# Kernel tuning notes

Hardware: AMD Instinct MI355X
Metric: run time of the kernel (lower is better)

## Reference

```python
import jax, jax.numpy as jnp
import numpy as np
import math

HIDDEN = 1024
NUM_HEADS = 16
HEAD_DIM = HIDDEN // NUM_HEADS


def _rope_tables(seq_len, dim, dtype):
    inv_freq = 1.0 / (10000.0 ** (np.arange(0, dim, 2, dtype=np.float32) / dim))
    t = np.arange(seq_len, dtype=np.float32)
    freqs = np.einsum('i,j->ij', t, inv_freq)          # [S, dim/2]
    emb = np.concatenate([freqs, freqs], axis=-1)      # [S, dim]
    return jnp.asarray(np.cos(emb), dtype), jnp.asarray(np.sin(emb), dtype)


def _rotate_half(x):
    x1, x2 = x[..., : x.shape[-1] // 2], x[..., x.shape[-1] // 2:]
    return jnp.concatenate([-x2, x1], axis=-1)


def setup_inputs() -> dict:
    key = jax.random.key(0)
    k1, k2, k3 = jax.random.split(key, 3)
    B, S = 2, 2048
    x = jax.random.normal(k1, (B, S, HIDDEN), dtype=jnp.float32)
    attention_mask = jnp.ones((B, S), dtype=jnp.int32)
    w_qkv = jax.random.normal(k2, (HIDDEN, 3 * HIDDEN), dtype=jnp.float32) * (1.0 / math.sqrt(HIDDEN))
    w_out = jax.random.normal(k3, (HIDDEN, HIDDEN), dtype=jnp.float32) * (1.0 / math.sqrt(HIDDEN))
    return {"x": x, "attention_mask": attention_mask, "w_qkv": w_qkv, "w_out": w_out}


def reference(x, attention_mask, w_qkv, w_out):
    B, S, H = x.shape
    qkv = x @ w_qkv                                   # [B,S,3H]
    qkv = qkv.reshape(B, S, NUM_HEADS, 3 * HEAD_DIM).transpose(0, 2, 1, 3)  # [B,h,S,3d]
    q, k, v = jnp.split(qkv, 3, axis=-1)              # each [B,h,S,d]
    cos, sin = _rope_tables(S, HEAD_DIM, x.dtype)     # [S,d]
    cos = cos[None, None]
    sin = sin[None, None]
    q = q * cos + _rotate_half(q) * sin
    k = k * cos + _rotate_half(k) * sin
    scale = math.sqrt(HEAD_DIM)
    scores = jnp.einsum('bhqd,bhkd->bhqk', q, k) / scale  # [B,h,S,S]
    mask_value = jnp.finfo(scores.dtype).min
    scores = jnp.where(attention_mask[:, None, None, :] == 0, mask_value, scores)
    attn = jax.nn.softmax(scores, axis=-1)
    context = jnp.einsum('bhqk,bhkd->bhqd', attn, v)  # [B,h,S,d]
    context = context.transpose(0, 2, 1, 3).reshape(B, S, H)
    return context @ w_out
```

## Files before the change

### kernel.cpp

```cpp
#include <hip/hip_runtime.h>
#include <hip/hip_bf16.h>
#include <math.h>
#include <stdint.h>


typedef __bf16 bf16;
typedef __bf16 bf16x8 __attribute__((ext_vector_type(8)));
typedef __bf16 bf16x4 __attribute__((ext_vector_type(4)));
typedef float f32x4 __attribute__((ext_vector_type(4)));

#define AS1 __attribute__((address_space(1)))
#define AS3 __attribute__((address_space(3)))

__device__ __forceinline__ void gload_lds16(const void* g, void* l) {
  __builtin_amdgcn_global_load_lds((const AS1 void*)g, (AS3 void*)l, 16, 0, 0);
}

__device__ __forceinline__ f32x4 mfma16(bf16x8 a, bf16x8 b, f32x4 c) {
  return __builtin_amdgcn_mfma_f32_16x16x32_bf16(a, b, c, 0, 0, 0);
}

#define S_LEN 2048
#define QSCALE 0.1803368801111144f


__global__ void k_split_x(const float* __restrict__ x, bf16* __restrict__ xh,
                          bf16* __restrict__ xl) {
  int i = blockIdx.x * 256 + threadIdx.x;
  float4 v = ((const float4*)x)[i];
  float vv[4] = {v.x, v.y, v.z, v.w};
  bf16x4 h, l;
#pragma unroll
  for (int j = 0; j < 4; j++) {
    bf16 hb = (bf16)vv[j];
    h[j] = hb;
    l[j] = (bf16)(vv[j] - (float)hb);
  }
  ((bf16x4*)xh)[i] = h;
  ((bf16x4*)xl)[i] = l;
}

__global__ void k_wt_qkv(const float* __restrict__ w, bf16* __restrict__ bth,
                         bf16* __restrict__ btl) {
  __shared__ float t[32][33];
  int n0 = blockIdx.x * 32, k0 = blockIdx.y * 32;
  int tx = threadIdx.x & 31, ty = threadIdx.x >> 5;
#pragma unroll
  for (int i = 0; i < 4; i++)
    t[ty + 8 * i][tx] = w[(size_t)(k0 + ty + 8 * i) * 3072 + n0 + tx];
  __syncthreads();
#pragma unroll
  for (int i = 0; i < 4; i++) {
    int r = ty + 8 * i;
    float v = t[tx][r];
    size_t o = (size_t)(n0 + r) * 1024 + k0 + tx;
    bf16 hb = (bf16)v;
    bth[o] = hb;
    btl[o] = (bf16)(v - (float)hb);
  }
}

__global__ void k_wt_out(const float* __restrict__ w, bf16* __restrict__ bt) {
  __shared__ float t[32][33];
  int n0 = blockIdx.x * 32, k0 = blockIdx.y * 32;
  int tx = threadIdx.x & 31, ty = threadIdx.x >> 5;
#pragma unroll
  for (int i = 0; i < 4; i++)
    t[ty + 8 * i][tx] = w[(size_t)(k0 + ty + 8 * i) * 1024 + n0 + tx];
  __syncthreads();
#pragma unroll
  for (int i = 0; i < 4; i++) {
    int r = ty + 8 * i;
    bt[(size_t)(n0 + r) * 1024 + k0 + tx] = (bf16)t[tx][r];
  }
}

__global__ void k_rope_tables(float* __restrict__ ct, float* __restrict__ st) {
  int i = blockIdx.x * 256 + threadIdx.x;
  int s = i >> 5, j = i & 31;
  double invf = pow(10000.0, -(double)j / 32.0);
  double a = (double)s * invf;
  ct[i] = (float)cos(a);
  st[i] = (float)sin(a);
}

__global__ __launch_bounds__(256, 2) void k_gemm_qkv(
    const bf16* __restrict__ Ah, const bf16* __restrict__ Al,
    const bf16* __restrict__ Bh, const bf16* __restrict__ Bl,
    bf16* __restrict__ C) {
  const int K = 1024, N = 3072;
  __shared__ __align__(16) bf16 sAh[128 * 32];
  __shared__ __align__(16) bf16 sAl[128 * 32];
  __shared__ __align__(16) bf16 sBh[128 * 32];
  __shared__ __align__(16) bf16 sBl[128 * 32];
  int tid = threadIdx.x, lane = tid & 63, wid = tid >> 6;
  int m0 = blockIdx.x * 128, n0 = blockIdx.y * 128;
  int wm = wid >> 1, wn = wid & 1;

  f32x4 acc[4][4];
#pragma unroll
  for (int a = 0; a < 4; a++)
#pragma unroll
    for (int b = 0; b < 4; b++) acc[a][b] = (f32x4){0.f, 0.f, 0.f, 0.f};

  for (int k0 = 0; k0 < K; k0 += 32) {
#pragma unroll
    for (int p = 0; p < 2; p++) {
      int slot = p * 256 + tid;
      int row = slot >> 2, c16 = slot & 3;
      int cs = c16 ^ ((row >> 1) & 3);
      int ldsoff = (p * 256 + wid * 64) * 16;
      size_t ga = (size_t)(m0 + row) * K + k0 + cs * 8;
      size_t gb = (size_t)(n0 + row) * K + k0 + cs * 8;
      gload_lds16(Ah + ga, (char*)sAh + ldsoff);
      gload_lds16(Al + ga, (char*)sAl + ldsoff);
      gload_lds16(Bh + gb, (char*)sBh + ldsoff);
      gload_lds16(Bl + gb, (char*)sBl + ldsoff);
    }
    __syncthreads();

    bf16x8 fah[4], fal[4], fbh[4], fbl[4];
#pragma unroll
    for (int mf = 0; mf < 4; mf++) {
      int row = wm * 64 + mf * 16 + (lane & 15);
      int c16 = (lane >> 4) ^ ((row >> 1) & 3);
      int off = row * 64 + c16 * 16;
      fah[mf] = *(const bf16x8*)((const char*)sAh + off);
      fal[mf] = *(const bf16x8*)((const char*)sAl + off);
    }
#pragma unroll
    for (int nf = 0; nf < 4; nf++) {
      int row = wn * 64 + nf * 16 + (lane & 15);
      int c16 = (lane >> 4) ^ ((row >> 1) & 3);
      int off = row * 64 + c16 * 16;
      fbh[nf] = *(const bf16x8*)((const char*)sBh + off);
      fbl[nf] = *(const bf16x8*)((const char*)sBl + off);
    }
#pragma unroll
    for (int mf = 0; mf < 4; mf++)
#pragma unroll
      for (int nf = 0; nf < 4; nf++) {
        acc[mf][nf] = mfma16(fah[mf], fbh[nf], acc[mf][nf]);
        acc[mf][nf] = mfma16(fah[mf], fbl[nf], acc[mf][nf]);
        acc[mf][nf] = mfma16(fal[mf], fbh[nf], acc[mf][nf]);
      }
    __syncthreads();
  }

#pragma unroll
  for (int mf = 0; mf < 4; mf++)
#pragma unroll
    for (int nf = 0; nf < 4; nf++)
#pragma unroll
      for (int r = 0; r < 4; r++) {
        int row = m0 + wm * 64 + mf * 16 + (lane >> 4) * 4 + r;
        int col = n0 + wn * 64 + nf * 16 + (lane & 15);
        C[(size_t)row * N + col] = (bf16)acc[mf][nf][r];
      }
}

__global__ void k_rope_scatter(const bf16* __restrict__ QKV,
                               const float* __restrict__ ct,
                               const float* __restrict__ st,
                               bf16* __restrict__ Q, bf16* __restrict__ Kb,
                               bf16* __restrict__ Vt) {
  __shared__ __align__(16) bf16 vt[64 * 64];
  int sblk = blockIdx.x, bh = blockIdx.y;
  int b = bh >> 4, h = bh & 15;
  int tid = threadIdx.x;
  int r = tid >> 2, c = tid & 3;
  int s = sblk * 64 + r;
  size_t rowbase = ((size_t)(b * S_LEN + s)) * 3072 + h * 192;

  bf16x8 qlo = *(const bf16x8*)(QKV + rowbase + c * 8);
  bf16x8 qhi = *(const bf16x8*)(QKV + rowbase + c * 8 + 32);
  bf16x8 klo = *(const bf16x8*)(QKV + rowbase + 64 + c * 8);
  bf16x8 khi = *(const bf16x8*)(QKV + rowbase + 64 + c * 8 + 32);
  bf16x8 vlo = *(const bf16x8*)(QKV + rowbase + 128 + c * 8);
  bf16x8 vhi = *(const bf16x8*)(QKV + rowbase + 128 + c * 8 + 32);

  bf16x8 qol, qoh, kol, koh;
#pragma unroll
  for (int j = 0; j < 8; j++) {
    float cs = ct[s * 32 + c * 8 + j], sn = st[s * 32 + c * 8 + j];
    float q1 = (float)qlo[j], q2 = (float)qhi[j];
    qol[j] = (bf16)((q1 * cs - q2 * sn) * QSCALE);
    qoh[j] = (bf16)((q2 * cs + q1 * sn) * QSCALE);
    float k1 = (float)klo[j], k2 = (float)khi[j];
    kol[j] = (bf16)(k1 * cs - k2 * sn);
    koh[j] = (bf16)(k2 * cs + k1 * sn);
  }
  size_t qb = ((size_t)bh * S_LEN + s) * 64 + c * 8;
  *(bf16x8*)(Q + qb) = qol;
  *(bf16x8*)(Q + qb + 32) = qoh;
  *(bf16x8*)(Kb + qb) = kol;
  *(bf16x8*)(Kb + qb + 32) = koh;

#pragma unroll
  for (int j = 0; j < 8; j++) {
    vt[(c * 8 + j) * 64 + r] = vlo[j];
    vt[(c * 8 + 32 + j) * 64 + r] = vhi[j];
  }
  __syncthreads();
  int d = tid >> 2, cc = tid & 3;
  size_t vb = ((size_t)bh * 64 + d) * S_LEN + sblk * 64 + cc * 16;
  *(bf16x8*)(Vt + vb) = *(const bf16x8*)(vt + d * 64 + cc * 16);
  *(bf16x8*)(Vt + vb + 8) = *(const bf16x8*)(vt + d * 64 + cc * 16 + 8);
}

__global__ __launch_bounds__(256, 2) void k_attn(
    const bf16* __restrict__ Q, const bf16* __restrict__ Kb,
    const bf16* __restrict__ Vt, const int* __restrict__ mask,
    bf16* __restrict__ Ctx) {
  __shared__ __align__(16) char sK[2][16384];
  __shared__ __align__(16) char sV[16384];
  int tid = threadIdx.x, lane = tid & 63, w = tid >> 6;
  int g = lane >> 4, q = lane & 15;
  int bh = blockIdx.x, qt = blockIdx.y;
  int b = bh >> 4, h = bh & 15;
  int q0 = qt * 128 + w * 32;

  bf16x8 bQ[2][2];
#pragma unroll
  for (int mf = 0; mf < 2; mf++)
#pragma unroll
    for (int ks = 0; ks < 2; ks++)
      bQ[mf][ks] = *(const bf16x8*)(Q + ((size_t)bh * S_LEN + q0 + mf * 16 + q) * 64 +
                                    ks * 32 + g * 8);

  f32x4 O[2][4];
  float mrow[2], lrow[2];
#pragma unroll
  for (int mf = 0; mf < 2; mf++) {
#pragma unroll
    for (int nd = 0; nd < 4; nd++) O[mf][nd] = (f32x4){0.f, 0.f, 0.f, 0.f};
    mrow[mf] = -3e38f;
    lrow[mf] = 0.f;
  }

  const bf16* kbase = Kb + (size_t)bh * S_LEN * 64;
  const bf16* vbase = Vt + (size_t)bh * 64 * S_LEN;

#pragma unroll
  for (int p = 0; p < 4; p++) {
    int slot = p * 256 + tid;
    int row = slot >> 3, c16 = slot & 7;
    int cs = c16 ^ (row & 7);
    gload_lds16(kbase + (size_t)row * 64 + cs * 8, sK[0] + (p * 256 + w * 64) * 16);
  }
  bf16x8 vst[4];
#pragma unroll
  for (int p = 0; p < 4; p++) {
    int slot = p * 256 + tid;
    int row = slot >> 4, c16 = slot & 15;
    int cs = c16 ^ (row & 7);
    vst[p] = *(const bf16x8*)(vbase + (size_t)row * S_LEN + cs * 8);
  }
#pragma unroll
  for (int p = 0; p < 4; p++)
    *(bf16x8*)(sV + (p * 256 + tid) * 16) = vst[p];
  __syncthreads();

  int db = 0;
  for (int kt = 0; kt < 16; kt++) {
    int k0 = kt * 128;
    if (kt < 15) {
#pragma unroll
      for (int p = 0; p < 4; p++) {
        int slot = p * 256 + tid;
        int row = slot >> 3, c16 = slot & 7;
        int cs = c16 ^ (row & 7);
        gload_lds16(kbase + (size_t)((kt + 1) * 128 + row) * 64 + cs * 8,
                    sK[db ^ 1] + (p * 256 + w * 64) * 16);
      }
#pragma unroll
      for (int p = 0; p < 4; p++) {
        int slot = p * 256 + tid;
        int row = slot >> 4, c16 = slot & 15;
        int cs = c16 ^ (row & 7);
        vst[p] = *(const bf16x8*)(vbase + (size_t)row * S_LEN + (kt + 1) * 128 + cs * 8);
      }
    }
    const char* kl = sK[db];

    f32x4 sfr[2][8];
#pragma unroll
    for (int mf = 0; mf < 2; mf++)
#pragma unroll
      for (int kf = 0; kf < 8; kf++) sfr[mf][kf] = (f32x4){0.f, 0.f, 0.f, 0.f};
#pragma unroll
    for (int kf = 0; kf < 8; kf++) {
#pragma unroll
      for (int ks = 0; ks < 2; ks++) {
        int row = kf * 16 + q;
        int c16 = (ks * 4 + g) ^ (row & 7);
        bf16x8 ak = *(const bf16x8*)(kl + row * 128 + c16 * 16);
        sfr[0][kf] = mfma16(ak, bQ[0][ks], sfr[0][kf]);
        sfr[1][kf] = mfma16(ak, bQ[1][ks], sfr[1][kf]);
      }
    }
    {
      int2 mv = *(const int2*)(mask + b * S_LEN + k0 + lane * 2);
      if (!__all(mv.x & mv.y)) {
#pragma unroll
        for (int kf = 0; kf < 8; kf++) {
          int4 m4 = *(const int4*)(mask + b * S_LEN + k0 + kf * 16 + g * 4);
          int mm[4] = {m4.x, m4.y, m4.z, m4.w};
#pragma unroll
          for (int r = 0; r < 4; r++)
            if (mm[r] == 0) { sfr[0][kf][r] = -1e30f; sfr[1][kf][r] = -1e30f; }
        }
      }
    }
#pragma unroll
    for (int mf = 0; mf < 2; mf++) {
      float mx = -3e38f;
#pragma unroll
      for (int kf = 0; kf < 8; kf++)
#pragma unroll
        for (int r = 0; r < 4; r++) mx = fmaxf(mx, sfr[mf][kf][r]);
      mx = fmaxf(mx, __shfl_xor(mx, 16, 64));
      mx = fmaxf(mx, __shfl_xor(mx, 32, 64));
      if (__any(mx > mrow[mf] + 8.0f)) {
        float mnew = fmaxf(mrow[mf], mx);
        float al = exp2f(mrow[mf] - mnew);
        mrow[mf] = mnew;
        lrow[mf] *= al;
#pragma unroll
        for (int nd = 0; nd < 4; nd++)
#pragma unroll
          for (int r = 0; r < 4; r++) O[mf][nd][r] *= al;
      }
      float ps = 0.f;
#pragma unroll
      for (int kf = 0; kf < 8; kf++)
#pragma unroll
        for (int r = 0; r < 4; r++) {
          float p0 = exp2f(sfr[mf][kf][r] - mrow[mf]);
          sfr[mf][kf][r] = p0;
          ps += p0;
        }
      ps += __shfl_xor(ps, 16, 64);
      ps += __shfl_xor(ps, 32, 64);
      lrow[mf] += ps;
    }

#pragma unroll
    for (int ks = 0; ks < 4; ks++) {
      bf16x8 pb[2];
#pragma unroll
      for (int mf = 0; mf < 2; mf++)
#pragma unroll
        for (int j = 0; j < 8; j++)
          pb[mf][j] = (bf16)sfr[mf][2 * ks + (j >> 2)][j & 3];
#pragma unroll
      for (int nd = 0; nd < 4; nd++) {
        int row = nd * 16 + q;
        int u1 = (ks * 4 + (g >> 1)) ^ (row & 7);
        int u2 = (ks * 4 + (g >> 1) + 2) ^ (row & 7);
        const char* vr = sV + row * 256 + ((g & 1) << 3);
        bf16x4 v0 = *(const bf16x4*)(vr + (u1 << 4));
        bf16x4 v1 = *(const bf16x4*)(vr + (u2 << 4));
        bf16x8 av;
#pragma unroll
        for (int j = 0; j < 4; j++) { av[j] = v0[j]; av[4 + j] = v1[j]; }
        O[0][nd] = mfma16(av, pb[0], O[0][nd]);
        O[1][nd] = mfma16(av, pb[1], O[1][nd]);
      }
    }
    __syncthreads();
    if (kt < 15) {
#pragma unroll
      for (int p = 0; p < 4; p++)
        *(bf16x8*)(sV + (p * 256 + tid) * 16) = vst[p];
    }
    __syncthreads();
    db ^= 1;
  }

#pragma unroll
  for (int mf = 0; mf < 2; mf++) {
    float inv = 1.f / lrow[mf];
    int srow = q0 + mf * 16 + q;
#pragma unroll
    for (int nd = 0; nd < 4; nd++) {
      bf16x4 o4;
#pragma unroll
      for (int r = 0; r < 4; r++) o4[r] = (bf16)(O[mf][nd][r] * inv);
      *(bf16x4*)(Ctx + ((size_t)b * S_LEN + srow) * 1024 + h * 64 + nd * 16 + g * 4) = o4;
    }
  }
}

__global__ __launch_bounds__(256, 2) void k_gemm_out(
    const bf16* __restrict__ A, const bf16* __restrict__ Bt,
    float* __restrict__ C) {
  const int K = 1024, N = 1024;
  __shared__ __align__(16) bf16 sA[128 * 32];
  __shared__ __align__(16) bf16 sB[128 * 32];
  int tid = threadIdx.x, lane = tid & 63, wid = tid >> 6;
  int m0 = blockIdx.x * 128, n0 = blockIdx.y * 128;
  int wm = wid >> 1, wn = wid & 1;

  f32x4 acc[4][4];
#pragma unroll
  for (int a = 0; a < 4; a++)
#pragma unroll
    for (int b = 0; b < 4; b++) acc[a][b] = (f32x4){0.f, 0.f, 0.f, 0.f};

  for (int k0 = 0; k0 < K; k0 += 32) {
#pragma unroll
    for (int p = 0; p < 2; p++) {
      int slot = p * 256 + tid;
      int row = slot >> 2, c16 = slot & 3;
      int cs = c16 ^ ((row >> 1) & 3);
      int ldsoff = (p * 256 + wid * 64) * 16;
      gload_lds16(A + (size_t)(m0 + row) * K + k0 + cs * 8, (char*)sA + ldsoff);
      gload_lds16(Bt + (size_t)(n0 + row) * K + k0 + cs * 8, (char*)sB + ldsoff);
    }
    __syncthreads();
    bf16x8 fa[4], fb[4];
#pragma unroll
    for (int mf = 0; mf < 4; mf++) {
      int row = wm * 64 + mf * 16 + (lane & 15);
      int c16 = (lane >> 4) ^ ((row >> 1) & 3);
      fa[mf] = *(const bf16x8*)((const char*)sA + row * 64 + c16 * 16);
    }
#pragma unroll
    for (int nf = 0; nf < 4; nf++) {
      int row = wn * 64 + nf * 16 + (lane & 15);
      int c16 = (lane >> 4) ^ ((row >> 1) & 3);
      fb[nf] = *(const bf16x8*)((const char*)sB + row * 64 + c16 * 16);
    }
#pragma unroll
    for (int mf = 0; mf < 4; mf++)
#pragma unroll
      for (int nf = 0; nf < 4; nf++)
        acc[mf][nf] = mfma16(fa[mf], fb[nf], acc[mf][nf]);
    __syncthreads();
  }
#pragma unroll
  for (int mf = 0; mf < 4; mf++)
#pragma unroll
    for (int nf = 0; nf < 4; nf++)
#pragma unroll
      for (int r = 0; r < 4; r++) {
        int row = m0 + wm * 64 + mf * 16 + (lane >> 4) * 4 + r;
        int col = n0 + wn * 64 + nf * 16 + (lane & 15);
        C[(size_t)row * N + col] = acc[mf][nf][r];
      }
}

extern "C" void kernel_launch(void* const* d_in, const int* in_sizes, int n_in,
                              void* d_out, int out_size, void* d_ws, size_t ws_size,
                              hipStream_t stream) {
  const float* x = (const float*)d_in[0];
  const int* mask = (const int*)d_in[1];
  const float* wqkv = (const float*)d_in[2];
  const float* wout = (const float*)d_in[3];
  float* out = (float*)d_out;
  char* ws = (char*)d_ws;

  bf16* Xh  = (bf16*)(ws + 0);
  bf16* Xl  = (bf16*)(ws + 8388608);
  bf16* Wqh = (bf16*)(ws + 16777216);
  bf16* Wql = (bf16*)(ws + 23068672);
  bf16* Wo  = (bf16*)(ws + 29360128);
  bf16* QKV = (bf16*)(ws + 31457280);
  bf16* Qb  = (bf16*)(ws + 56623104);
  bf16* Kb  = (bf16*)(ws + 65011712);
  bf16* Vt  = (bf16*)(ws + 73400320);
  bf16* Ctx = (bf16*)(ws + 81788928);
  float* ct = (float*)(ws + 90177536);
  float* st = (float*)(ws + 90439680);

  k_split_x<<<4096, 256, 0, stream>>>(x, Xh, Xl);
  k_wt_qkv<<<dim3(96, 32), 256, 0, stream>>>(wqkv, Wqh, Wql);
  k_wt_out<<<dim3(32, 32), 256, 0, stream>>>(wout, Wo);
  k_rope_tables<<<256, 256, 0, stream>>>(ct, st);
  k_gemm_qkv<<<dim3(32, 24), 256, 0, stream>>>(Xh, Xl, Wqh, Wql, QKV);
  k_rope_scatter<<<dim3(32, 32), 256, 0, stream>>>(QKV, ct, st, Qb, Kb, Vt);
  k_attn<<<dim3(32, 16), 256, 0, stream>>>(Qb, Kb, Vt, mask, Ctx);
  k_gemm_out<<<dim3(32, 8), 256, 0, stream>>>(Ctx, Wo, out);
}
```

Measured before the change: 259.8 us.

## Double-buffer V tile in attention, hoist LDS offsets and mask check

The attention kernel now double-buffers the V tile in shared memory alongside K. This removes one __syncthreads per key tile, since the next V tile is written into the other buffer. LDS read offsets and global load pointers are precomputed once, and the all-ones mask test is done once per block instead of every tile. The rope table kernel is also switched from double to float math. The cost is 64KB of LDS per block, which may limit the two-blocks-per-CU occupancy on the hardware, plus more registers held for the offset tables.

Result: no change. 259.5 us (-0.1%).

```diff
diff --git a/kernel.cpp b/kernel.cpp
--- a/kernel.cpp
+++ b/kernel.cpp
@@ -78,10 +78,10 @@
 __global__ void k_rope_tables(float* __restrict__ ct, float* __restrict__ st) {
   int i = blockIdx.x * 256 + threadIdx.x;
   int s = i >> 5, j = i & 31;
-  double invf = pow(10000.0, -(double)j / 32.0);
-  double a = (double)s * invf;
-  ct[i] = (float)cos(a);
-  st[i] = (float)sin(a);
+  float invf = powf(10000.0f, -(float)j / 32.0f);
+  float a = (float)s * invf;
+  ct[i] = cosf(a);
+  st[i] = sinf(a);
 }
 
 __global__ __launch_bounds__(256, 2) void k_gemm_qkv(
@@ -212,8 +212,9 @@
     const bf16* __restrict__ Q, const bf16* __restrict__ Kb,
     const bf16* __restrict__ Vt, const int* __restrict__ mask,
     bf16* __restrict__ Ctx) {
-  __shared__ __align__(16) char sK[2][16384];
-  __shared__ __align__(16) char sV[16384];
+  __shared__ __align__(16) char sKV[65536];
+  char* sKbase = sKV;
+  char* sVbase = sKV + 32768;
   int tid = threadIdx.x, lane = tid & 63, w = tid >> 6;
   int g = lane >> 4, q = lane & 15;
   int bh = blockIdx.x, qt = blockIdx.y;
@@ -238,15 +239,62 @@
     lrow[mf] = 0.f;
   }
 
+  bool rowall;
+  {
+    int acc = -1;
+    const int4* mr = (const int4*)(mask + (size_t)b * S_LEN) + lane * 8;
+#pragma unroll
+    for (int p = 0; p < 8; p++) {
+      int4 m4 = mr[p];
+      acc &= m4.x & m4.y & m4.z & m4.w;
+    }
+    rowall = __all(acc != 0);
+  }
+
   const bf16* kbase = Kb + (size_t)bh * S_LEN * 64;
   const bf16* vbase = Vt + (size_t)bh * 64 * S_LEN;
+
+  const bf16* kgp[4];
+  const bf16* vgp[4];
+  int kldo[4], vldo[4];
+#pragma unroll
+  for (int p = 0; p < 4; p++) {
+    int slot = p * 256 + tid;
+    int krow = slot >> 3, kc = slot & 7;
+    int kcs = kc ^ (krow & 7);
+    kgp[p] = kbase + (size_t)(128 + krow) * 64 + kcs * 8;
+    kldo[p] = (p * 256 + w * 64) * 16;
+    int vrow = slot >> 4, vc = slot & 15;
+    int vcs = vc ^ (vrow & 7);
+    vgp[p] = vbase + (size_t)vrow * S_LEN + 128 + vcs * 8;
+    vldo[p] = (p * 256 + tid) * 16;
+  }
+  int koff[8][2];
+#pragma unroll
+  for (int kf = 0; kf < 8; kf++)
+#pragma unroll
+    for (int ks = 0; ks < 2; ks++) {
+      int row = kf * 16 + q;
+      koff[kf][ks] = row * 128 + (((ks * 4 + g) ^ (row & 7)) << 4);
+    }
+  int voff[4][4][2];
+#pragma unroll
+  for (int ks = 0; ks < 4; ks++)
+#pragma unroll
+    for (int nd = 0; nd < 4; nd++) {
+      int row = nd * 16 + q;
+      int u1 = (ks * 4 + (g >> 1)) ^ (row & 7);
+      int u2 = (ks * 4 + (g >> 1) + 2) ^ (row & 7);
+      voff[ks][nd][0] = row * 256 + ((g & 1) << 3) + (u1 << 4);
+      voff[ks][nd][1] = row * 256 + ((g & 1) << 3) + (u2 << 4);
+    }
 
 #pragma unroll
   for (int p = 0; p < 4; p++) {
     int slot = p * 256 + tid;
     int row = slot >> 3, c16 = slot & 7;
     int cs = c16 ^ (row & 7);
-    gload_lds16(kbase + (size_t)row * 64 + cs * 8, sK[0] + (p * 256 + w * 64) * 16);
+    gload_lds16(kbase + (size_t)row * 64 + cs * 8, sKbase + kldo[p]);
   }
   bf16x8 vst[4];
 #pragma unroll
@@ -258,30 +306,26 @@
   }
 #pragma unroll
   for (int p = 0; p < 4; p++)
-    *(bf16x8*)(sV + (p * 256 + tid) * 16) = vst[p];
+    *(bf16x8*)(sVbase + vldo[p]) = vst[p];
   __syncthreads();
 
   int db = 0;
   for (int kt = 0; kt < 16; kt++) {
-    int k0 = kt * 128;
     if (kt < 15) {
+      char* kdst = sKbase + (db ^ 1) * 16384;
 #pragma unroll
       for (int p = 0; p < 4; p++) {
-        int slot = p * 256 + tid;
-        int row = slot >> 3, c16 = slot & 7;
-        int cs = c16 ^ (row & 7);
-        gload_lds16(kbase + (size_t)((kt + 1) * 128 + row) * 64 + cs * 8,
-                    sK[db ^ 1] + (p * 256 + w * 64) * 16);
+        gload_lds16(kgp[p], kdst + kldo[p]);
+        kgp[p] += 128 * 64;
       }
 #pragma unroll
       for (int p = 0; p < 4; p++) {
-        int slot = p * 256 + tid;
-        int row = slot >> 4, c16 = slot & 15;
-        int cs = c16 ^ (row & 7);
-        vst[p] = *(const bf16x8*)(vbase + (size_t)row * S_LEN + (kt + 1) * 128 + cs * 8);
-      }
-    }
-    const char* kl = sK[db];
+        vst[p] = *(const bf16x8*)vgp[p];
+        vgp[p] += 128;
+      }
+    }
+    const char* kl = sKbase + db * 16384;
+    const char* vl = sVbase + db * 16384;
 
     f32x4 sfr[2][8];
 #pragma unroll
@@ -292,24 +336,20 @@
     for (int kf = 0; kf < 8; kf++) {
 #pragma unroll
       for (int ks = 0; ks < 2; ks++) {
-        int row = kf * 16 + q;
-        int c16 = (ks * 4 + g) ^ (row & 7);
-        bf16x8 ak = *(const bf16x8*)(kl + row * 128 + c16 * 16);
+        bf16x8 ak = *(const bf16x8*)(kl + koff[kf][ks]);
         sfr[0][kf] = mfma16(ak, bQ[0][ks], sfr[0][kf]);
         sfr[1][kf] = mfma16(ak, bQ[1][ks], sfr[1][kf]);
       }
     }
-    {
-      int2 mv = *(const int2*)(mask + b * S_LEN + k0 + lane * 2);
-      if (!__all(mv.x & mv.y)) {
-#pragma unroll
-        for (int kf = 0; kf < 8; kf++) {
-          int4 m4 = *(const int4*)(mask + b * S_LEN + k0 + kf * 16 + g * 4);
-          int mm[4] = {m4.x, m4.y, m4.z, m4.w};
-#pragma unroll
-          for (int r = 0; r < 4; r++)
-            if (mm[r] == 0) { sfr[0][kf][r] = -1e30f; sfr[1][kf][r] = -1e30f; }
-        }
+    if (!rowall) {
+      int k0 = kt * 128;
+#pragma unroll
+      for (int kf = 0; kf < 8; kf++) {
+        int4 m4 = *(const int4*)(mask + b * S_LEN + k0 + kf * 16 + g * 4);
+        int mm[4] = {m4.x, m4.y, m4.z, m4.w};
+#pragma unroll
+        for (int r = 0; r < 4; r++)
+          if (mm[r] == 0) { sfr[0][kf][r] = -1e30f; sfr[1][kf][r] = -1e30f; }
       }
     }
 #pragma unroll
@@ -355,12 +395,8 @@
           pb[mf][j] = (bf16)sfr[mf][2 * ks + (j >> 2)][j & 3];
 #pragma unroll
       for (int nd = 0; nd < 4; nd++) {
-        int row = nd * 16 + q;
-        int u1 = (ks * 4 + (g >> 1)) ^ (row & 7);
-        int u2 = (ks * 4 + (g >> 1) + 2) ^ (row & 7);
-        const char* vr = sV + row * 256 + ((g & 1) << 3);
-        bf16x4 v0 = *(const bf16x4*)(vr + (u1 << 4));
-        bf16x4 v1 = *(const bf16x4*)(vr + (u2 << 4));
+        bf16x4 v0 = *(const bf16x4*)(vl + voff[ks][nd][0]);
+        bf16x4 v1 = *(const bf16x4*)(vl + voff[ks][nd][1]);
         bf16x8 av;
 #pragma unroll
         for (int j = 0; j < 4; j++) { av[j] = v0[j]; av[4 + j] = v1[j]; }
@@ -368,11 +404,11 @@
         O[1][nd] = mfma16(av, pb[1], O[1][nd]);
       }
     }
-    __syncthreads();
     if (kt < 15) {
+      char* vdst = sVbase + (db ^ 1) * 16384;
 #pragma unroll
       for (int p = 0; p < 4; p++)
-        *(bf16x8*)(sV + (p * 256 + tid) * 16) = vst[p];
+        *(bf16x8*)(vdst + vldo[p]) = vst[p];
     }
     __syncthreads();
     db ^= 1;
```
